# Kernel tuning notes

Hardware: AMD Instinct MI355X
Metric: run time of the kernel (lower is better)

## Reference

```python
import jax, jax.numpy as jnp
import numpy as np

B, S, D, H, E, K, HID = 4, 1024, 1024, 16, 8, 2, 4096
HD = D // H


def _ln(x, g, b):
    m = x.mean(-1, keepdims=True)
    v = x.var(-1, keepdims=True)
    return (x - m) / jnp.sqrt(v + 1e-5) * g + b


def setup_inputs():
    key = jax.random.key(0)
    ks = jax.random.split(key, 12)
    p = lambda i, shape: jax.random.normal(ks[i], shape, jnp.float32) * 0.02
    return {
        "x": jax.random.normal(ks[0], (B, S, D), jnp.float32),
        "text_state": jax.random.normal(ks[1], (B, D), jnp.float32),
        "ln1_g": jnp.ones((D,), jnp.float32), "ln1_b": jnp.zeros((D,), jnp.float32),
        "wqkv": p(2, (D, 3 * D)), "bqkv": jnp.zeros((3 * D,), jnp.float32),
        "wo": p(3, (D, D)), "bo": jnp.zeros((D,), jnp.float32),
        "rel_bias": p(4, (H, 2 * S - 1)),
        "ln2_g": jnp.ones((D,), jnp.float32), "ln2_b": jnp.zeros((D,), jnp.float32),
        "cap_w": p(5, (D, D)), "cap_b": jnp.zeros((D,), jnp.float32),
        "gate_w": p(6, (D, E)), "gate_b": jnp.zeros((E,), jnp.float32),
        "w1": p(7, (E, D, HID)), "b1": jnp.zeros((E, HID), jnp.float32),
        "w2": p(8, (E, HID, D)), "b2": jnp.zeros((E, D), jnp.float32),
    }


def reference(x, text_state, ln1_g, ln1_b, wqkv, bqkv, wo, bo, rel_bias,
              ln2_g, ln2_b, cap_w, cap_b, gate_w, gate_b, w1, b1, w2, b2):
    # --- temporal-bias multi-head self-attention (pre-LN, residual) ---
    h = _ln(x, ln1_g, ln1_b)
    qkv = h @ wqkv + bqkv                          # [B,S,3D]
    q, k, v = jnp.split(qkv, 3, axis=-1)
    q = q.reshape(B, S, H, HD).transpose(0, 2, 1, 3)
    k = k.reshape(B, S, H, HD).transpose(0, 2, 1, 3)
    v = v.reshape(B, S, H, HD).transpose(0, 2, 1, 3)
    scores = jnp.einsum('bhqd,bhkd->bhqk', q, k) / jnp.sqrt(jnp.float32(HD))
    rel = jnp.arange(S)[:, None] - jnp.arange(S)[None, :] + (S - 1)  # [S,S]
    scores = scores + rel_bias[:, rel][None]       # learned temporal bias per head
    attn = jax.nn.softmax(scores, axis=-1)
    o = jnp.einsum('bhqk,bhkd->bhqd', attn, v).transpose(0, 2, 1, 3).reshape(B, S, D)
    x = x + o @ wo + bo

    # --- caption-conditioned top-k MoE FFN (pre-LN, residual) ---
    h2 = _ln(x, ln2_g, ln2_b)
    gate_in = h2 + (text_state @ cap_w + cap_b)[:, None, :]
    logits = gate_in @ gate_w + gate_b             # [B,S,E]
    vals, eidx = jax.lax.top_k(logits, K)          # [B,S,K]
    gw = jax.nn.softmax(vals, axis=-1)
    y = jnp.einsum('bsd,edh->bseh', h2, w1) + b1   # all experts densely
    y = jax.nn.gelu(y)
    y = jnp.einsum('bseh,ehd->bsed', y, w2) + b2   # [B,S,E,D]
    sel = jnp.take_along_axis(y, eidx[..., None], axis=2)  # [B,S,K,D]
    moe = (gw[..., None] * sel).sum(axis=2)
    x = x + moe

    load = jnp.mean(jax.nn.one_hot(eidx, E, dtype=jnp.float32), axis=(0, 1, 2))
    return x, load
```

## Files before the change

kernel.cpp:

```cpp
#include <hip/hip_runtime.h>
#include <hip/hip_bf16.h>

typedef __attribute__((ext_vector_type(8))) short short8;
typedef __attribute__((ext_vector_type(4))) float f32x4;

#define MFMA16(a,b,c) __builtin_amdgcn_mfma_f32_16x16x32_bf16((a),(b),(c),0,0,0)

__device__ __forceinline__ short f2b(float f){
    return __builtin_bit_cast(short, __float2bfloat16(f));
}
__device__ __forceinline__ void split2(float f, short &hi, short &lo){
    __hip_bfloat16 h = __float2bfloat16(f);
    hi = __builtin_bit_cast(short, h);
    lo = f2b(f - __bfloat162float(h));
}
__device__ __forceinline__ void cp16(void* l, const void* g){
    __builtin_amdgcn_global_load_lds(
        (const __attribute__((address_space(1))) unsigned int*)g,
        (__attribute__((address_space(3))) unsigned int*)l, 16, 0, 0);
}

__global__ __launch_bounds__(256)
void castT_k(const float* __restrict__ in, short* __restrict__ hiT,
             short* __restrict__ loT, int R, int C)
{
    __shared__ float t[64][65];
    size_t boff = (size_t)blockIdx.z * (size_t)R * (size_t)C;
    int r0 = blockIdx.y * 64, c0 = blockIdx.x * 64;
    int tid = threadIdx.x;
    int lr = tid >> 4, lc = (tid & 15) * 4;
#pragma unroll
    for (int p = 0; p < 4; p++) {
        int r = p*16 + lr;
        float4 v = *reinterpret_cast<const float4*>(in + boff + (size_t)(r0+r)*C + c0 + lc);
        t[r][lc] = v.x; t[r][lc+1] = v.y; t[r][lc+2] = v.z; t[r][lc+3] = v.w;
    }
    __syncthreads();
#pragma unroll
    for (int p = 0; p < 2; p++) {
        int ch = p*256 + tid;
        int c = ch >> 3, seg = (ch & 7) * 8;
        short8 hv, lv;
#pragma unroll
        for (int i = 0; i < 8; i++) {
            float v = t[seg+i][c];
            short h, l; split2(v, h, l);
            hv[i] = h; lv[i] = l;
        }
        size_t o = boff + (size_t)(c0+c)*R + r0 + seg;
        *reinterpret_cast<short8*>(hiT + o) = hv;
        if (loT) *reinterpret_cast<short8*>(loT + o) = lv;
    }
}

__global__ __launch_bounds__(256)
void ln_k(const float* __restrict__ x, const float* __restrict__ g,
          const float* __restrict__ be, short* __restrict__ outhi,
          short* __restrict__ outlo)
{
    int row = blockIdx.x;
    const float* xr = x + (size_t)row * 1024;
    int tid = threadIdx.x;
    float4 v = reinterpret_cast<const float4*>(xr)[tid];
    float s = v.x + v.y + v.z + v.w;
    float q = v.x*v.x + v.y*v.y + v.z*v.z + v.w*v.w;
#pragma unroll
    for (int m = 1; m < 64; m <<= 1) { s += __shfl_xor(s, m); q += __shfl_xor(q, m); }
    __shared__ float ss[4], sq[4];
    int wid = tid >> 6;
    if ((tid & 63) == 0) { ss[wid] = s; sq[wid] = q; }
    __syncthreads();
    float S = ss[0] + ss[1] + ss[2] + ss[3];
    float Qs = sq[0] + sq[1] + sq[2] + sq[3];
    float mean = S * (1.f/1024.f);
    float var = Qs * (1.f/1024.f) - mean*mean;
    float rstd = rsqrtf(var + 1e-5f);
    float4 gv = reinterpret_cast<const float4*>(g)[tid];
    float4 bv = reinterpret_cast<const float4*>(be)[tid];
    float o[4];
    o[0] = (v.x-mean)*rstd*gv.x + bv.x;
    o[1] = (v.y-mean)*rstd*gv.y + bv.y;
    o[2] = (v.z-mean)*rstd*gv.z + bv.z;
    o[3] = (v.w-mean)*rstd*gv.w + bv.w;
    short hs[4], ls[4];
#pragma unroll
    for (int i = 0; i < 4; i++) split2(o[i], hs[i], ls[i]);
    typedef __attribute__((ext_vector_type(4))) short short4v;
    short4v hv; hv[0]=hs[0]; hv[1]=hs[1]; hv[2]=hs[2]; hv[3]=hs[3];
    *reinterpret_cast<short4v*>(outhi + (size_t)row*1024 + tid*4) = hv;
    if (outlo) {
        short4v lv; lv[0]=ls[0]; lv[1]=ls[1]; lv[2]=ls[2]; lv[3]=ls[3];
        *reinterpret_cast<short4v*>(outlo + (size_t)row*1024 + tid*4) = lv;
    }
}

__global__ __launch_bounds__(256)
void cap_k(const float* __restrict__ ts, const float* __restrict__ cw,
           const float* __restrict__ cb, float* __restrict__ capo)
{
    int b = blockIdx.y;
    int d = blockIdx.x * 64 + (threadIdx.x & 63);
    int ks = threadIdx.x >> 6;
    const float* t = ts + (size_t)b * 1024;
    float acc = 0.f;
    for (int k = ks*256; k < ks*256 + 256; k++)
        acc = fmaf(t[k], cw[(size_t)k*1024 + d], acc);
    __shared__ float red[4][64];
    red[ks][threadIdx.x & 63] = acc;
    __syncthreads();
    if (ks == 0)
        capo[(size_t)b*1024 + d] = red[0][threadIdx.x&63] + red[1][threadIdx.x&63]
                                 + red[2][threadIdx.x&63] + red[3][threadIdx.x&63] + cb[d];
}

__global__ __launch_bounds__(64)
void gate_k(const float* __restrict__ x2, const float* __restrict__ g,
            const float* __restrict__ be, const float* __restrict__ capo,
            const float* __restrict__ gw, const float* __restrict__ gb,
            int* __restrict__ elist, float* __restrict__ ewt, int* __restrict__ cnt)
{
    int t = blockIdx.x;
    int b = t >> 10;
    int lane = threadIdx.x;
    const float* xr = x2 + (size_t)t * 1024;
    float v[16];
    float s = 0.f, q = 0.f;
#pragma unroll
    for (int i = 0; i < 16; i++) {
        v[i] = xr[i*64 + lane];
        s += v[i]; q += v[i]*v[i];
    }
#pragma unroll
    for (int m = 1; m < 64; m <<= 1) { s += __shfl_xor(s, m); q += __shfl_xor(q, m); }
    float mean = s * (1.f/1024.f);
    float var = q * (1.f/1024.f) - mean*mean;
    float rstd = rsqrtf(var + 1e-5f);
    float acc[8] = {0,0,0,0,0,0,0,0};
    const float* cr = capo + (size_t)b * 1024;
#pragma unroll
    for (int i = 0; i < 16; i++) {
        int d = i*64 + lane;
        float gi = (v[i]-mean)*rstd*g[d] + be[d] + cr[d];
        const float4* gp = reinterpret_cast<const float4*>(gw + (size_t)d*8);
        float4 g0 = gp[0], g1 = gp[1];
        acc[0] += gi*g0.x; acc[1] += gi*g0.y; acc[2] += gi*g0.z; acc[3] += gi*g0.w;
        acc[4] += gi*g1.x; acc[5] += gi*g1.y; acc[6] += gi*g1.z; acc[7] += gi*g1.w;
    }
#pragma unroll
    for (int e = 0; e < 8; e++)
#pragma unroll
        for (int m = 1; m < 64; m <<= 1) acc[e] += __shfl_xor(acc[e], m);
    if (lane == 0) {
        float v0 = -1e30f, v1 = -1e30f; int i0 = 0, i1 = 0;
#pragma unroll
        for (int e = 0; e < 8; e++) {
            float lg = acc[e] + gb[e];
            if (lg > v0) { v1 = v0; i1 = i0; v0 = lg; i0 = e; }
            else if (lg > v1) { v1 = lg; i1 = e; }
        }
        float w0 = 1.f / (1.f + __expf(v1 - v0));
        float w1 = 1.f - w0;
        int p0 = atomicAdd(&cnt[i0], 1);
        elist[i0*4096 + p0] = t; ewt[i0*4096 + p0] = w0;
        int p1 = atomicAdd(&cnt[i1], 1);
        elist[i1*4096 + p1] = t; ewt[i1*4096 + p1] = w1;
    }
}

__global__ void scan_k(const int* __restrict__ cnt, int* __restrict__ ebase,
                       float* __restrict__ outload)
{
    int t = threadIdx.x;
    if (t == 0) { int s = 0; for (int e = 0; e < 8; e++) { ebase[e] = s; s += cnt[e]; } }
    if (t < 8) outload[t] = (float)cnt[t] * (1.f/8192.f);
}

enum { M_QKV = 0, M_WO = 1, M_F1 = 2, M_F2 = 3 };

template<int MODE, bool SP>
__global__ __launch_bounds__(256)
void gemm_k(const short* __restrict__ Ahi, const short* __restrict__ Alo,
            const short* __restrict__ Bhi, const short* __restrict__ Blo,
            const float* __restrict__ bias,
            float* __restrict__ outf, short* __restrict__ outhi,
            const float* __restrict__ resid,
            const int* __restrict__ elist, const float* __restrict__ ew,
            const int* __restrict__ cnt, const int* __restrict__ ebase,
            int M, int N, int K)
{
    constexpr int NT = SP ? 4 : 2;
    constexpr bool MOE = (MODE == M_F1 || MODE == M_F2);
    int e = blockIdx.z;
    int m0 = blockIdx.y * 128, n0 = blockIdx.x * 128;
    int Mloc = M;
    int baseE = 0;
    if (MOE) {
        Mloc = cnt[e];
        if (m0 >= Mloc) return;
        baseE = ebase[e];
        Bhi += (size_t)e * 4194304;
        bias += (size_t)e * N;
    }
    __shared__ short lds[NT * 8192];
    int* rowmap = nullptr;
    if constexpr (MOE) {
        __shared__ int rowmap_s[128];
        rowmap = rowmap_s;
    }
    int tid = threadIdx.x;
    int lane = tid & 63, wid = tid >> 6;
    int wr = wid >> 1, wc = wid & 1;
    int rl = lane & 15, rg = lane >> 4;

    if constexpr (MOE) {
        if (tid < 128) {
            int mrow = m0 + tid;
            int ar;
            if (MODE == M_F1) {
                int idx = mrow < Mloc ? mrow : Mloc - 1;
                ar = elist[e*4096 + idx];
            } else {
                ar = baseE + mrow;
                if (ar > 8191) ar = 8191;
            }
            rowmap[tid] = ar;
        }
        __syncthreads();
    }

    auto STAGE = [&](int buf, int k0) {
        short* base = lds + buf * (NT * 4096);
        for (int is = wid; is < NT * 8; is += 4) {
            int tile = is >> 3, issue = is & 7;
            int row = issue*16 + (lane >> 2);
            int sch = (lane & 3) ^ ((row >> 1) & 3);
            const short* src;
            if (tile < (SP ? 2 : 1)) {
                int ar = MOE ? rowmap[row] : (m0 + row);
                const short* Ab = (SP && tile == 1) ? Alo : Ahi;
                src = Ab + (size_t)ar * K + k0 + sch*8;
            } else {
                const short* Bb = (SP && tile == 3) ? Blo : Bhi;
                src = Bb + (size_t)(n0 + row) * K + k0 + sch*8;
            }
            cp16(base + tile*4096 + issue*512, src);
        }
    };

    f32x4 acc[4][4] = {};
    int nt = K >> 5;
    STAGE(0, 0);
    int cur = 0;
    for (int t = 0; t < nt; ++t) {
        __syncthreads();
        if (t + 1 < nt) STAGE(cur ^ 1, (t + 1) * 32);
        const short* cb = lds + cur * (NT * 4096);
        short8 afh[4], bfh[4], afl[4], bfl[4];
#pragma unroll
        for (int i = 0; i < 4; i++) {
            int ra = wr*64 + i*16 + rl;
            int ca = ra*32 + ((rg ^ ((ra >> 1) & 3)) * 8);
            afh[i] = *reinterpret_cast<const short8*>(cb + ca);
            if (SP) afl[i] = *reinterpret_cast<const short8*>(cb + 4096 + ca);
            int rb = wc*64 + i*16 + rl;
            int cb2 = rb*32 + ((rg ^ ((rb >> 1) & 3)) * 8);
            bfh[i] = *reinterpret_cast<const short8*>(cb + (SP?2:1)*4096 + cb2);
            if (SP) bfl[i] = *reinterpret_cast<const short8*>(cb + 3*4096 + cb2);
        }
#pragma unroll
        for (int mi = 0; mi < 4; mi++)
#pragma unroll
            for (int ni = 0; ni < 4; ni++) {
                acc[mi][ni] = MFMA16(afh[mi], bfh[ni], acc[mi][ni]);
                if (SP) {
                    acc[mi][ni] = MFMA16(afh[mi], bfl[ni], acc[mi][ni]);
                    acc[mi][ni] = MFMA16(afl[mi], bfh[ni], acc[mi][ni]);
                }
            }
        cur ^= 1;
    }
#pragma unroll
    for (int mi = 0; mi < 4; mi++) {
#pragma unroll
        for (int ni = 0; ni < 4; ni++) {
            int col = n0 + wc*64 + ni*16 + rl;
            f32x4 a = acc[mi][ni];
#pragma unroll
            for (int r = 0; r < 4; r++) {
                int mrow = m0 + wr*64 + mi*16 + rg*4 + r;
                if (mrow >= Mloc) continue;
                float val = a[r] + bias[col];
                if (MODE == M_QKV) {
                    int which = col >> 10, d = col & 1023;
                    int hh = d >> 6, hd = d & 63;
                    int bb = mrow >> 10, sidx = mrow & 1023;
                    size_t o = (size_t)which*4194304 + (((size_t)(bb*16 + hh))*1024 + sidx)*64 + hd;
                    short h, l; split2(val, h, l);
                    outhi[o] = h; outhi[12582912 + o] = l;
                } else if (MODE == M_WO) {
                    size_t o = (size_t)mrow*1024 + col;
                    outf[o] = val + resid[o];
                } else if (MODE == M_F1) {
                    float xx = val;
                    float z = 0.7978845608028654f * (xx + 0.044715f*xx*xx*xx);
                    float th = 1.f - 2.f/(1.f + __expf(2.f*z));
                    float gl = 0.5f*xx*(1.f + th);
                    outhi[(size_t)(baseE + mrow)*4096 + col] = f2b(gl);
                } else {
                    int tok = elist[e*4096 + mrow];
                    float w = ew[e*4096 + mrow];
                    atomicAdd(&outf[(size_t)tok*1024 + col], w*val);
                }
            }
        }
    }
}

__global__ __launch_bounds__(256)
void attn_k(const short* __restrict__ qkvhi, const short* __restrict__ qkvlo,
            const float* __restrict__ relb,
            short* __restrict__ obhi, short* __restrict__ oblo)
{
    int bh = blockIdx.y, qt = blockIdx.x;
    int b = bh >> 4, h = bh & 15;
    int tid = threadIdx.x, wid = tid >> 6, lane = tid & 63;
    int rl = lane & 15, rg = lane >> 4;
    const short* Qh = qkvhi + (size_t)bh * 65536;
    const short* Ql = qkvlo + (size_t)bh * 65536;
    const short* Kh_g = qkvhi + 4194304 + (size_t)bh * 65536;
    const short* Kl_g = qkvlo + 4194304 + (size_t)bh * 65536;
    const short* Vh_g = qkvhi + 8388608 + (size_t)bh * 65536;
    const short* Vl_g = qkvlo + 8388608 + (size_t)bh * 65536;
    __shared__ short Kh[64][72], Kl[64][72];
    __shared__ short Vh[64][72], Vl[64][72];
    __shared__ short Ph[4][16][72], Pl[4][16][72];
    int q0 = qt*64 + wid*16;
    short8 qh0 = *reinterpret_cast<const short8*>(Qh + (size_t)(q0+rl)*64 + rg*8);
    short8 qh1 = *reinterpret_cast<const short8*>(Qh + (size_t)(q0+rl)*64 + 32 + rg*8);
    short8 ql0 = *reinterpret_cast<const short8*>(Ql + (size_t)(q0+rl)*64 + rg*8);
    short8 ql1 = *reinterpret_cast<const short8*>(Ql + (size_t)(q0+rl)*64 + 32 + rg*8);
    f32x4 O[4] = {};
    float mr[4] = {-1e30f,-1e30f,-1e30f,-1e30f};
    float lr[4] = {0.f,0.f,0.f,0.f};
    const float* rb = relb + h*2047 + 1023;
    for (int kt = 0; kt < 16; ++kt) {
        int kb0 = kt * 64;
        __syncthreads();
#pragma unroll
        for (int j = 0; j < 2; j++) {
            int idx = j*256 + tid;
            int row = idx >> 3, cb = (idx & 7) * 8;
            *reinterpret_cast<short8*>(&Kh[row][cb]) =
                *reinterpret_cast<const short8*>(Kh_g + (size_t)(kb0+row)*64 + cb);
            *reinterpret_cast<short8*>(&Kl[row][cb]) =
                *reinterpret_cast<const short8*>(Kl_g + (size_t)(kb0+row)*64 + cb);
            short8 vh = *reinterpret_cast<const short8*>(Vh_g + (size_t)(kb0+row)*64 + cb);
            short8 vl = *reinterpret_cast<const short8*>(Vl_g + (size_t)(kb0+row)*64 + cb);
#pragma unroll
            for (int i = 0; i < 8; i++) { Vh[cb+i][row] = vh[i]; Vl[cb+i][row] = vl[i]; }
        }
        __syncthreads();
        f32x4 sc[4];
#pragma unroll
        for (int c = 0; c < 4; c++) {
            short8 kh0 = *reinterpret_cast<short8*>(&Kh[c*16+rl][rg*8]);
            short8 kh1 = *reinterpret_cast<short8*>(&Kh[c*16+rl][32+rg*8]);
            short8 kl0 = *reinterpret_cast<short8*>(&Kl[c*16+rl][rg*8]);
            short8 kl1 = *reinterpret_cast<short8*>(&Kl[c*16+rl][32+rg*8]);
            f32x4 t = {};
            t = MFMA16(qh0, kh0, t); t = MFMA16(qh1, kh1, t);
            t = MFMA16(qh0, kl0, t); t = MFMA16(qh1, kl1, t);
            t = MFMA16(ql0, kh0, t); t = MFMA16(ql1, kh1, t);
            sc[c] = t;
        }
        float pm[4] = {-1e30f,-1e30f,-1e30f,-1e30f};
#pragma unroll
        for (int c = 0; c < 4; c++) {
            int kk = kb0 + c*16 + rl;
#pragma unroll
            for (int r = 0; r < 4; r++) {
                int q = q0 + rg*4 + r;
                float sv = sc[c][r]*0.125f + rb[q - kk];
                sc[c][r] = sv;
                pm[r] = fmaxf(pm[r], sv);
            }
        }
#pragma unroll
        for (int r = 0; r < 4; r++) {
            pm[r] = fmaxf(pm[r], __shfl_xor(pm[r], 1));
            pm[r] = fmaxf(pm[r], __shfl_xor(pm[r], 2));
            pm[r] = fmaxf(pm[r], __shfl_xor(pm[r], 4));
            pm[r] = fmaxf(pm[r], __shfl_xor(pm[r], 8));
        }
        float scl[4], ps[4];
#pragma unroll
        for (int r = 0; r < 4; r++) {
            float mn = fmaxf(mr[r], pm[r]);
            scl[r] = __expf(mr[r] - mn);
            mr[r] = mn;
            ps[r] = 0.f;
        }
#pragma unroll
        for (int c = 0; c < 4; c++)
#pragma unroll
            for (int r = 0; r < 4; r++) {
                float p = __expf(sc[c][r] - mr[r]);
                sc[c][r] = p;
                ps[r] += p;
            }
#pragma unroll
        for (int r = 0; r < 4; r++) {
            ps[r] += __shfl_xor(ps[r], 1);
            ps[r] += __shfl_xor(ps[r], 2);
            ps[r] += __shfl_xor(ps[r], 4);
            ps[r] += __shfl_xor(ps[r], 8);
            lr[r] = lr[r]*scl[r] + ps[r];
        }
#pragma unroll
        for (int cc = 0; cc < 4; cc++) {
            O[cc][0] *= scl[0]; O[cc][1] *= scl[1];
            O[cc][2] *= scl[2]; O[cc][3] *= scl[3];
        }
#pragma unroll
        for (int c = 0; c < 4; c++)
#pragma unroll
            for (int r = 0; r < 4; r++) {
                short hp, lp; split2(sc[c][r], hp, lp);
                Ph[wid][rg*4+r][c*16+rl] = hp;
                Pl[wid][rg*4+r][c*16+rl] = lp;
            }
#pragma unroll
        for (int cc = 0; cc < 4; cc++) {
#pragma unroll
            for (int ks = 0; ks < 2; ks++) {
                short8 ph = *reinterpret_cast<short8*>(&Ph[wid][rl][ks*32 + rg*8]);
                short8 pl = *reinterpret_cast<short8*>(&Pl[wid][rl][ks*32 + rg*8]);
                short8 vh = *reinterpret_cast<short8*>(&Vh[cc*16+rl][ks*32 + rg*8]);
                short8 vl = *reinterpret_cast<short8*>(&Vl[cc*16+rl][ks*32 + rg*8]);
                O[cc] = MFMA16(ph, vh, O[cc]);
                O[cc] = MFMA16(ph, vl, O[cc]);
                O[cc] = MFMA16(pl, vh, O[cc]);
            }
        }
    }
#pragma unroll
    for (int cc = 0; cc < 4; cc++) {
#pragma unroll
        for (int r = 0; r < 4; r++) {
            int q = q0 + rg*4 + r;
            float val = O[cc][r] / lr[r];
            size_t o = ((size_t)(b*1024 + q))*1024 + h*64 + cc*16 + rl;
            short hv, lv; split2(val, hv, lv);
            obhi[o] = hv; oblo[o] = lv;
        }
    }
}

extern "C" void kernel_launch(void* const* d_in, const int* in_sizes, int n_in,
                              void* d_out, int out_size, void* d_ws, size_t ws_size,
                              hipStream_t stream)
{
    const float* x     = (const float*)d_in[0];
    const float* ts    = (const float*)d_in[1];
    const float* ln1g  = (const float*)d_in[2];
    const float* ln1b_ = (const float*)d_in[3];
    const float* wqkv  = (const float*)d_in[4];
    const float* bqkv  = (const float*)d_in[5];
    const float* wo    = (const float*)d_in[6];
    const float* bo    = (const float*)d_in[7];
    const float* relb  = (const float*)d_in[8];
    const float* ln2g  = (const float*)d_in[9];
    const float* ln2b_ = (const float*)d_in[10];
    const float* capw  = (const float*)d_in[11];
    const float* capb  = (const float*)d_in[12];
    const float* gatew = (const float*)d_in[13];
    const float* gateb = (const float*)d_in[14];
    const float* w1    = (const float*)d_in[15];
    const float* b1    = (const float*)d_in[16];
    const float* w2    = (const float*)d_in[17];
    const float* b2    = (const float*)d_in[18];
    float* out = (float*)d_out;

    char* p = (char*)d_ws;
    short* w1T    = (short*)p; p += 67108864;
    short* w2T    = (short*)p; p += 67108864;
    short* wqThi  = (short*)p; p += 6291456;
    short* wqTlo  = (short*)p; p += 6291456;
    short* woThi  = (short*)p; p += 2097152;
    short* woTlo  = (short*)p; p += 2097152;
    short* qkvhi  = (short*)p; p += 25165824;
    short* qkvlo  = qkvhi + 12582912; p += 0;
    p += 25165824 - 25165824;
    p = (char*)(qkvhi + 25165824);
    short* h2b    = (short*)p; p += 8388608;
    float* capo   = (float*)p; p += 16384;
    int*   elist  = (int*)p;   p += 131072;
    float* ewt    = (float*)p; p += 131072;
    int*   cnt    = (int*)p;   p += 256;
    int*   ebase  = (int*)p;   p += 256;
    short* mid    = (short*)p; p += 67108864;
    short* h1hi   = mid;
    short* h1lo   = mid + 4194304;
    short* obhi   = mid + 8388608;
    short* oblo   = mid + 12582912;

    hipMemsetAsync(cnt, 0, 32, stream);

    castT_k<<<dim3(48, 16, 1), 256, 0, stream>>>(wqkv, wqThi, wqTlo, 1024, 3072);
    castT_k<<<dim3(16, 16, 1), 256, 0, stream>>>(wo,   woThi, woTlo, 1024, 1024);
    castT_k<<<dim3(64, 16, 8), 256, 0, stream>>>(w1,   w1T,  nullptr, 1024, 4096);
    castT_k<<<dim3(16, 64, 8), 256, 0, stream>>>(w2,   w2T,  nullptr, 4096, 1024);

    ln_k<<<4096, 256, 0, stream>>>(x, ln1g, ln1b_, h1hi, h1lo);

    gemm_k<M_QKV, true><<<dim3(24, 32, 1), 256, 0, stream>>>(
        h1hi, h1lo, wqThi, wqTlo, bqkv, nullptr, qkvhi,
        nullptr, nullptr, nullptr, nullptr, nullptr, 4096, 3072, 1024);

    attn_k<<<dim3(16, 64), 256, 0, stream>>>(qkvhi, qkvlo, relb, obhi, oblo);

    gemm_k<M_WO, true><<<dim3(8, 32, 1), 256, 0, stream>>>(
        obhi, oblo, woThi, woTlo, bo, out, nullptr,
        x, nullptr, nullptr, nullptr, nullptr, 4096, 1024, 1024);

    cap_k<<<dim3(16, 4), 256, 0, stream>>>(ts, capw, capb, capo);

    ln_k<<<4096, 256, 0, stream>>>(out, ln2g, ln2b_, h2b, nullptr);

    gate_k<<<4096, 64, 0, stream>>>(out, ln2g, ln2b_, capo, gatew, gateb,
                                    elist, ewt, cnt);

    scan_k<<<1, 64, 0, stream>>>(cnt, ebase, out + 4194304);

    gemm_k<M_F1, false><<<dim3(32, 32, 8), 256, 0, stream>>>(
        h2b, nullptr, w1T, nullptr, b1, nullptr, mid,
        nullptr, elist, ewt, cnt, ebase, 4096, 4096, 1024);

    gemm_k<M_F2, false><<<dim3(8, 32, 8), 256, 0, stream>>>(
        mid, nullptr, w2T, nullptr, b2, out, nullptr,
        nullptr, elist, ewt, cnt, ebase, 4096, 1024, 4096);

    (void)in_sizes; (void)n_in; (void)out_size; (void)ws_size;
}
```

Baseline: 1.409 ms.

## Switch GEMM to single-buffered LDS with precomputed per-thread load pointers

The GEMM drops the double-buffered LDS pipeline. Each k-step now loads into a single buffer, synchronises, computes, and synchronises again. Per-thread global source pointers are computed once and advanced by a fixed stride, which removes per-iteration address and rowmap work, and LDS use is halved so more blocks can be resident per CU. The cost is that global-to-LDS copies no longer overlap MFMA work within a block, so the kernel depends on occupancy to hide latency. The GEMM is also wrapped in non-template kernel entry points, and the workspace pointer arithmetic is tidied.

```diff
diff --git a/kernel.cpp b/kernel.cpp
--- a/kernel.cpp
+++ b/kernel.cpp
@@ -178,17 +178,18 @@
 enum { M_QKV = 0, M_WO = 1, M_F1 = 2, M_F2 = 3 };
 
 template<int MODE, bool SP>
-__global__ __launch_bounds__(256)
-void gemm_k(const short* __restrict__ Ahi, const short* __restrict__ Alo,
-            const short* __restrict__ Bhi, const short* __restrict__ Blo,
-            const float* __restrict__ bias,
-            float* __restrict__ outf, short* __restrict__ outhi,
-            const float* __restrict__ resid,
-            const int* __restrict__ elist, const float* __restrict__ ew,
-            const int* __restrict__ cnt, const int* __restrict__ ebase,
-            int M, int N, int K)
+__device__ __forceinline__
+void gemm_body(const short* __restrict__ Ahi, const short* __restrict__ Alo,
+               const short* __restrict__ Bhi, const short* __restrict__ Blo,
+               const float* __restrict__ bias,
+               float* __restrict__ outf, short* __restrict__ outhi,
+               const float* __restrict__ resid,
+               const int* __restrict__ elist, const float* __restrict__ ew,
+               const int* __restrict__ cnt, const int* __restrict__ ebase,
+               int M, int N, int K)
 {
     constexpr int NT = SP ? 4 : 2;
+    constexpr int IPW = NT * 2;
     constexpr bool MOE = (MODE == M_F1 || MODE == M_F2);
     int e = blockIdx.z;
     int m0 = blockIdx.y * 128, n0 = blockIdx.x * 128;
@@ -201,7 +202,7 @@
         Bhi += (size_t)e * 4194304;
         bias += (size_t)e * N;
     }
-    __shared__ short lds[NT * 8192];
+    __shared__ short lds[NT * 4096];
     int* rowmap = nullptr;
     if constexpr (MOE) {
         __shared__ int rowmap_s[128];
@@ -228,44 +229,45 @@
         __syncthreads();
     }
 
-    auto STAGE = [&](int buf, int k0) {
-        short* base = lds + buf * (NT * 4096);
-        for (int is = wid; is < NT * 8; is += 4) {
-            int tile = is >> 3, issue = is & 7;
-            int row = issue*16 + (lane >> 2);
-            int sch = (lane & 3) ^ ((row >> 1) & 3);
-            const short* src;
-            if (tile < (SP ? 2 : 1)) {
-                int ar = MOE ? rowmap[row] : (m0 + row);
-                const short* Ab = (SP && tile == 1) ? Alo : Ahi;
-                src = Ab + (size_t)ar * K + k0 + sch*8;
-            } else {
-                const short* Bb = (SP && tile == 3) ? Blo : Bhi;
-                src = Bb + (size_t)(n0 + row) * K + k0 + sch*8;
-            }
-            cp16(base + tile*4096 + issue*512, src);
-        }
-    };
+    int sch = (lane & 3) ^ ((lane >> 3) & 3);
+    const short* src[IPW];
+#pragma unroll
+    for (int j = 0; j < IPW; j++) {
+        int g = wid * IPW + j;
+        int tile = g >> 3, iss = g & 7;
+        int row = iss*16 + (lane >> 2);
+        const short* base;
+        size_t ar;
+        if (tile < (SP ? 2 : 1)) {
+            ar = MOE ? (size_t)rowmap[row] : (size_t)(m0 + row);
+            base = (SP && tile == 1) ? Alo : Ahi;
+        } else {
+            ar = (size_t)(n0 + row);
+            base = (SP && tile == 3) ? Blo : Bhi;
+        }
+        src[j] = base + ar * (size_t)K + sch*8;
+    }
 
     f32x4 acc[4][4] = {};
     int nt = K >> 5;
-    STAGE(0, 0);
-    int cur = 0;
     for (int t = 0; t < nt; ++t) {
+#pragma unroll
+        for (int j = 0; j < IPW; j++) {
+            cp16(lds + (wid*IPW + j)*512, src[j]);
+            src[j] += 32;
+        }
         __syncthreads();
-        if (t + 1 < nt) STAGE(cur ^ 1, (t + 1) * 32);
-        const short* cb = lds + cur * (NT * 4096);
         short8 afh[4], bfh[4], afl[4], bfl[4];
 #pragma unroll
         for (int i = 0; i < 4; i++) {
             int ra = wr*64 + i*16 + rl;
-            int ca = ra*32 + ((rg ^ ((ra >> 1) & 3)) * 8);
-            afh[i] = *reinterpret_cast<const short8*>(cb + ca);
-            if (SP) afl[i] = *reinterpret_cast<const short8*>(cb + 4096 + ca);
+            int ca = ra*32 + ((rg ^ ((rl >> 1) & 3)) * 8);
+            afh[i] = *reinterpret_cast<const short8*>(lds + ca);
+            if (SP) afl[i] = *reinterpret_cast<const short8*>(lds + 4096 + ca);
             int rb = wc*64 + i*16 + rl;
-            int cb2 = rb*32 + ((rg ^ ((rb >> 1) & 3)) * 8);
-            bfh[i] = *reinterpret_cast<const short8*>(cb + (SP?2:1)*4096 + cb2);
-            if (SP) bfl[i] = *reinterpret_cast<const short8*>(cb + 3*4096 + cb2);
+            int cb2 = rb*32 + ((rg ^ ((rl >> 1) & 3)) * 8);
+            bfh[i] = *reinterpret_cast<const short8*>(lds + (SP?2:1)*4096 + cb2);
+            if (SP) bfl[i] = *reinterpret_cast<const short8*>(lds + 3*4096 + cb2);
         }
 #pragma unroll
         for (int mi = 0; mi < 4; mi++)
@@ -277,7 +279,7 @@
                     acc[mi][ni] = MFMA16(afl[mi], bfh[ni], acc[mi][ni]);
                 }
             }
-        cur ^= 1;
+        __syncthreads();
     }
 #pragma unroll
     for (int mi = 0; mi < 4; mi++) {
@@ -316,6 +318,16 @@
     }
 }
 
+#define GEMM_ARGS const short* Ahi, const short* Alo, const short* Bhi, const short* Blo, \
+    const float* bias, float* outf, short* outhi, const float* resid, \
+    const int* elist, const float* ew, const int* cnt, const int* ebase, int M, int N, int K
+#define GEMM_PASS Ahi, Alo, Bhi, Blo, bias, outf, outhi, resid, elist, ew, cnt, ebase, M, N, K
+
+__global__ __launch_bounds__(256) void gemmQKV_k(GEMM_ARGS){ gemm_body<M_QKV,true >(GEMM_PASS); }
+__global__ __launch_bounds__(256) void gemmWO_k (GEMM_ARGS){ gemm_body<M_WO, true >(GEMM_PASS); }
+__global__ __launch_bounds__(256) void gemmF1_k (GEMM_ARGS){ gemm_body<M_F1, false>(GEMM_PASS); }
+__global__ __launch_bounds__(256) void gemmF2_k (GEMM_ARGS){ gemm_body<M_F2, false>(GEMM_PASS); }
+
 __global__ __launch_bounds__(256)
 void attn_k(const short* __restrict__ qkvhi, const short* __restrict__ qkvlo,
             const float* __restrict__ relb,
@@ -488,10 +500,8 @@
     short* wqTlo  = (short*)p; p += 6291456;
     short* woThi  = (short*)p; p += 2097152;
     short* woTlo  = (short*)p; p += 2097152;
-    short* qkvhi  = (short*)p; p += 25165824;
-    short* qkvlo  = qkvhi + 12582912; p += 0;
-    p += 25165824 - 25165824;
-    p = (char*)(qkvhi + 25165824);
+    short* qkvhi  = (short*)p; p += 50331648;
+    short* qkvlo  = qkvhi + 12582912;
     short* h2b    = (short*)p; p += 8388608;
     float* capo   = (float*)p; p += 16384;
     int*   elist  = (int*)p;   p += 131072;
@@ -513,13 +523,13 @@
 
     ln_k<<<4096, 256, 0, stream>>>(x, ln1g, ln1b_, h1hi, h1lo);
 
-    gemm_k<M_QKV, true><<<dim3(24, 32, 1), 256, 0, stream>>>(
+    gemmQKV_k<<<dim3(24, 32, 1), 256, 0, stream>>>(
         h1hi, h1lo, wqThi, wqTlo, bqkv, nullptr, qkvhi,
         nullptr, nullptr, nullptr, nullptr, nullptr, 4096, 3072, 1024);
 
     attn_k<<<dim3(16, 64), 256, 0, stream>>>(qkvhi, qkvlo, relb, obhi, oblo);
 
-    gemm_k<M_WO, true><<<dim3(8, 32, 1), 256, 0, stream>>>(
+    gemmWO_k<<<dim3(8, 32, 1), 256, 0, stream>>>(
         obhi, oblo, woThi, woTlo, bo, out, nullptr,
         x, nullptr, nullptr, nullptr, nullptr, 4096, 1024, 1024);
 
@@ -532,11 +542,11 @@
 
     scan_k<<<1, 64, 0, stream>>>(cnt, ebase, out + 4194304);
 
-    gemm_k<M_F1, false><<<dim3(32, 32, 8), 256, 0, stream>>>(
+    gemmF1_k<<<dim3(32, 32, 8), 256, 0, stream>>>(
         h2b, nullptr, w1T, nullptr, b1, nullptr, mid,
         nullptr, elist, ewt, cnt, ebase, 4096, 4096, 1024);
 
-    gemm_k<M_F2, false><<<dim3(8, 32, 8), 256, 0, stream>>>(
+    gemmF2_k<<<dim3(8, 32, 8), 256, 0, stream>>>(
         mid, nullptr, w2T, nullptr, b2, out, nullptr,
         nullptr, elist, ewt, cnt, ebase, 4096, 1024, 4096);
 
```

Result: faster. 1.128 ms (-20.0%).
